# Kernel optimization log

Measured on AMD Instinct MI355X. Metric: run time of the kernel, lower is better.

The kernel has to match this reference:

```python
import jax, jax.numpy as jnp
import numpy as np

EPS = 1e-6
QMAX = 127.0  # 8-bit absmax activation quantization (BitNet b1.58 style)


def _quant_weight(W):
    # ternary {-1,0,1} with per-tensor mean-abs scale
    scale = jnp.mean(jnp.abs(W))
    scale = jnp.maximum(scale, EPS)
    q = jnp.clip(jnp.round(W / scale), -1.0, 1.0)
    return q * scale  # dequantized ternary weight


def _quant_act(x):
    # per-token absmax 8-bit quantization over the feature dim
    s = QMAX / jnp.maximum(jnp.max(jnp.abs(x), axis=-1, keepdims=True), EPS)
    q = jnp.clip(jnp.round(x * s), -QMAX - 1.0, QMAX)
    return q / s  # dequantized activation


def setup_inputs() -> dict:
    key = jax.random.key(0)
    k1, k2 = jax.random.split(key)
    B, S, D_IN, D_OUT = 4, 2048, 4096, 4096
    x = jax.random.normal(k1, (B, S, D_IN), dtype=jnp.float32)
    # xavier-uniform-ish weight init
    limit = float(np.sqrt(6.0 / (D_IN + D_OUT)))
    W = jax.random.uniform(k2, (D_OUT, D_IN), dtype=jnp.float32, minval=-limit, maxval=limit)
    b = jnp.zeros((D_OUT,), dtype=jnp.float32)
    return {"x": x, "W": W, "b": b}


def reference(x, W, b):
    dqx = _quant_act(x)      # [B,S,Din]
    dqw = _quant_weight(W)   # [Dout,Din]
    # F.linear: x @ W.T + b
    out = jnp.einsum('bsd,od->bso', dqx, dqw) + b
    return out
```

## Files before the change

kernel.cpp:

```cpp
#include <hip/hip_runtime.h>
#include <hip/hip_bf16.h>
#include <stdint.h>
#include <stddef.h>

#define DIN   4096
#define DOUT  4096
#define MTOK  8192
#define NW4   4194304

typedef __attribute__((ext_vector_type(4))) int   i32x4;
typedef __attribute__((ext_vector_type(4))) float f32x4;

#define OFF_SUM 0
#define OFF_WS  8
#define OFF_F   256
#define OFF_QX  65536
#define OFF_QW  (65536 + 8192*4096)

__global__ __launch_bounds__(256) void k_sumabs(const float* __restrict__ W,
                                                double* __restrict__ sum) {
  int idx = blockIdx.x * 256 + threadIdx.x;
  const f32x4* W4 = (const f32x4*)W;
  double s = 0.0;
#pragma unroll
  for (int i = 0; i < 8; ++i) {
    f32x4 v = W4[idx + i * 524288];
    s += (double)fabsf(v[0]);
    s += (double)fabsf(v[1]);
    s += (double)fabsf(v[2]);
    s += (double)fabsf(v[3]);
  }
#pragma unroll
  for (int off = 32; off > 0; off >>= 1) s += __shfl_xor(s, off);
  __shared__ double wsum[4];
  int lane = threadIdx.x & 63, w = threadIdx.x >> 6;
  if (lane == 0) wsum[w] = s;
  __syncthreads();
  if (threadIdx.x == 0) atomicAdd(sum, wsum[0] + wsum[1] + wsum[2] + wsum[3]);
}

__global__ void k_wscale(const double* __restrict__ sum, float* __restrict__ wsc) {
  double mean = *sum / 16777216.0;
  float s = (float)mean;
  if (s < 1e-6f) s = 1e-6f;
  *wsc = s;
}

__global__ __launch_bounds__(256) void k_quantw(const float* __restrict__ W,
                                                const float* __restrict__ wsc,
                                                char* __restrict__ qW) {
  int idx = blockIdx.x * 256 + threadIdx.x;
  float s = *wsc;
  f32x4 v = ((const f32x4*)W)[idx];
  int q0 = (int)fminf(fmaxf(rintf(v[0] / s), -1.f), 1.f);
  int q1 = (int)fminf(fmaxf(rintf(v[1] / s), -1.f), 1.f);
  int q2 = (int)fminf(fmaxf(rintf(v[2] / s), -1.f), 1.f);
  int q3 = (int)fminf(fmaxf(rintf(v[3] / s), -1.f), 1.f);
  uint32_t packed = (uint32_t)(q0 & 255) | ((uint32_t)(q1 & 255) << 8) |
                    ((uint32_t)(q2 & 255) << 16) | ((uint32_t)(q3 & 255) << 24);
  ((uint32_t*)qW)[idx] = packed;
}

__global__ __launch_bounds__(256) void k_quantx(const float* __restrict__ x,
                                                const float* __restrict__ wsc,
                                                char* __restrict__ qX,
                                                float* __restrict__ f) {
  int tok = blockIdx.x;
  int t = threadIdx.x;
  const f32x4* xr = (const f32x4*)(x + (size_t)tok * DIN);
  f32x4 v[4];
  float m = 0.f;
#pragma unroll
  for (int i = 0; i < 4; ++i) {
    v[i] = xr[t + 256 * i];
    m = fmaxf(m, fmaxf(fmaxf(fabsf(v[i][0]), fabsf(v[i][1])),
                       fmaxf(fabsf(v[i][2]), fabsf(v[i][3]))));
  }
#pragma unroll
  for (int off = 32; off > 0; off >>= 1) m = fmaxf(m, __shfl_xor(m, off));
  __shared__ float wm[4];
  if ((t & 63) == 0) wm[t >> 6] = m;
  __syncthreads();
  m = fmaxf(fmaxf(wm[0], wm[1]), fmaxf(wm[2], wm[3]));
  m = fmaxf(m, 1e-6f);
  float s = 127.0f / m;
  uint32_t* qr = (uint32_t*)(qX + (size_t)tok * DIN);
#pragma unroll
  for (int i = 0; i < 4; ++i) {
    int q0 = (int)fminf(fmaxf(rintf(v[i][0] * s), -128.f), 127.f);
    int q1 = (int)fminf(fmaxf(rintf(v[i][1] * s), -128.f), 127.f);
    int q2 = (int)fminf(fmaxf(rintf(v[i][2] * s), -128.f), 127.f);
    int q3 = (int)fminf(fmaxf(rintf(v[i][3] * s), -128.f), 127.f);
    uint32_t packed = (uint32_t)(q0 & 255) | ((uint32_t)(q1 & 255) << 8) |
                      ((uint32_t)(q2 & 255) << 16) | ((uint32_t)(q3 & 255) << 24);
    qr[t + 256 * i] = packed;
  }
  if (t == 0) f[tok] = (*wsc) * (m / 127.0f);
}

#define BM 128
#define BN 128
#define BK 64

__device__ __forceinline__ void gload16(const void* g, void* l) {
  __builtin_amdgcn_global_load_lds(
      (const __attribute__((address_space(1))) void*)g,
      (__attribute__((address_space(3))) void*)l, 16, 0, 0);
}

__global__ __launch_bounds__(256) void k_gemm(const char* __restrict__ qX,
                                              const char* __restrict__ qW,
                                              const float* __restrict__ f,
                                              const float* __restrict__ bias,
                                              float* __restrict__ out) {
  int bid = blockIdx.x;
  int swz = (bid & 7) * 256 + (bid >> 3);
  int bmi = swz >> 5;
  int bni = swz & 31;
  int bm0 = bmi * BM, bn0 = bni * BN;

  __shared__ char smem[16384];

  const int t = threadIdx.x;
  const int lane = t & 63;
  const int w = t >> 6;
  const int wm = w >> 1, wn = w & 1;

  i32x4 acc[4][4] = {};

  const int rs = t >> 2;
  const int cs = (t & 3) << 4;
  const char* srcA = qX + (size_t)(bm0 + rs) * DIN + cs;
  const char* srcB = qW + (size_t)(bn0 + rs) * DIN + cs;
  char* dstA0 = smem + w * 1024;
  char* dstA1 = smem + 4096 + w * 1024;
  char* dstB0 = smem + 8192 + w * 1024;
  char* dstB1 = smem + 12288 + w * 1024;

  const char* baseA = smem + (size_t)(wm * 64 + (lane & 15)) * 64 + ((lane >> 4) << 4);
  const char* baseB = smem + 8192 + (size_t)(wn * 64 + (lane & 15)) * 64 + ((lane >> 4) << 4);

  for (int kt = 0; kt < DIN / BK; ++kt) {
    const int k0 = kt * BK;
    gload16(srcA + k0, dstA0);
    gload16(srcA + (size_t)64 * DIN + k0, dstA1);
    gload16(srcB + k0, dstB0);
    gload16(srcB + (size_t)64 * DIN + k0, dstB1);
    __syncthreads();

    i32x4 a[4], b[4];
#pragma unroll
    for (int i = 0; i < 4; ++i) a[i] = *(const i32x4*)(baseA + i * 16 * 64);
#pragma unroll
    for (int j = 0; j < 4; ++j) b[j] = *(const i32x4*)(baseB + j * 16 * 64);
#pragma unroll
    for (int i = 0; i < 4; ++i)
#pragma unroll
      for (int j = 0; j < 4; ++j)
        acc[i][j] = __builtin_amdgcn_mfma_i32_16x16x64_i8(a[i], b[j], acc[i][j], 0, 0, 0);
    __syncthreads();
  }

  const int col0 = bn0 + wn * 64 + (lane & 15);
  const int row0 = bm0 + wm * 64 + ((lane >> 4) << 2);
  float bj[4];
#pragma unroll
  for (int j = 0; j < 4; ++j) bj[j] = bias[col0 + j * 16];
#pragma unroll
  for (int i = 0; i < 4; ++i) {
#pragma unroll
    for (int q = 0; q < 4; ++q) {
      const int m = row0 + i * 16 + q;
      const float fm = f[m];
      float* orow = out + (size_t)m * DOUT;
#pragma unroll
      for (int j = 0; j < 4; ++j)
        orow[col0 + j * 16] = (float)acc[i][j][q] * fm + bj[j];
    }
  }
}

extern "C" void kernel_launch(void* const* d_in, const int* in_sizes, int n_in,
                              void* d_out, int out_size, void* d_ws, size_t ws_size,
                              hipStream_t stream) {
  const float* x    = (const float*)d_in[0];
  const float* W    = (const float*)d_in[1];
  const float* bias = (const float*)d_in[2];
  float* out = (float*)d_out;
  char* ws = (char*)d_ws;

  double* sum = (double*)(ws + OFF_SUM);
  float* wsc  = (float*)(ws + OFF_WS);
  float* f    = (float*)(ws + OFF_F);
  char* qX    = ws + OFF_QX;
  char* qW    = ws + OFF_QW;

  hipMemsetAsync(d_ws, 0, 256, stream);
  k_sumabs<<<2048, 256, 0, stream>>>(W, sum);
  k_wscale<<<1, 1, 0, stream>>>(sum, wsc);
  k_quantw<<<16384, 256, 0, stream>>>(W, wsc, qW);
  k_quantx<<<8192, 256, 0, stream>>>(x, wsc, qX, f);
  k_gemm<<<2048, 256, 0, stream>>>(qX, qW, f, bias, out);
}
```

Baseline: 450.0 us.

## Merge quant kernels, pre-tile int8 operands, and pipeline a 256x256 int8 GEMM

Replaces the separate weight-scale, weight-quant and activation-quant kernels with one k_quant kernel. It folds in the weight-scale computation and writes qX and qW in a pre-tiled 16-row by 64-byte layout, so each GEMM stage is a contiguous 1 KB load per wave. The GEMM moves to 512-thread blocks with 256x256 output tiles and a 4-deep LDS ring buffer filled by global_load_lds. It uses vmcnt-based waits, a single barrier per k-step, MFMA priority hints and an XCD-aware block mapping, and applies the weight scale in the epilogue. The aim is fewer launches, more operand reuse and better load/compute overlap, at the cost of 128 KB of LDS per block and more registers per thread.

Result: no change. 450.1 us (+0.0%).

```diff
diff --git a/kernel.cpp b/kernel.cpp
--- a/kernel.cpp
+++ b/kernel.cpp
@@ -3,19 +3,19 @@
 #include <stdint.h>
 #include <stddef.h>
 
-#define DIN   4096
-#define DOUT  4096
-#define MTOK  8192
-#define NW4   4194304
+#define DIN  4096
+#define MTOK 8192
+#define NOUT 4096
+#define KT   64
 
 typedef __attribute__((ext_vector_type(4))) int   i32x4;
 typedef __attribute__((ext_vector_type(4))) float f32x4;
 
 #define OFF_SUM 0
-#define OFF_WS  8
 #define OFF_F   256
 #define OFF_QX  65536
-#define OFF_QW  (65536 + 8192*4096)
+#define OFF_QW  (65536 + (size_t)MTOK*DIN)
+
 
 __global__ __launch_bounds__(256) void k_sumabs(const float* __restrict__ W,
                                                 double* __restrict__ sum) {
@@ -25,10 +25,8 @@
 #pragma unroll
   for (int i = 0; i < 8; ++i) {
     f32x4 v = W4[idx + i * 524288];
-    s += (double)fabsf(v[0]);
-    s += (double)fabsf(v[1]);
-    s += (double)fabsf(v[2]);
-    s += (double)fabsf(v[3]);
+    s += (double)fabsf(v[0]) + (double)fabsf(v[1]) +
+         (double)fabsf(v[2]) + (double)fabsf(v[3]);
   }
 #pragma unroll
   for (int off = 32; off > 0; off >>= 1) s += __shfl_xor(s, off);
@@ -39,68 +37,88 @@
   if (threadIdx.x == 0) atomicAdd(sum, wsum[0] + wsum[1] + wsum[2] + wsum[3]);
 }
 
-__global__ void k_wscale(const double* __restrict__ sum, float* __restrict__ wsc) {
-  double mean = *sum / 16777216.0;
-  float s = (float)mean;
-  if (s < 1e-6f) s = 1e-6f;
-  *wsc = s;
-}
-
-__global__ __launch_bounds__(256) void k_quantw(const float* __restrict__ W,
-                                                const float* __restrict__ wsc,
-                                                char* __restrict__ qW) {
-  int idx = blockIdx.x * 256 + threadIdx.x;
-  float s = *wsc;
-  f32x4 v = ((const f32x4*)W)[idx];
-  int q0 = (int)fminf(fmaxf(rintf(v[0] / s), -1.f), 1.f);
-  int q1 = (int)fminf(fmaxf(rintf(v[1] / s), -1.f), 1.f);
-  int q2 = (int)fminf(fmaxf(rintf(v[2] / s), -1.f), 1.f);
-  int q3 = (int)fminf(fmaxf(rintf(v[3] / s), -1.f), 1.f);
-  uint32_t packed = (uint32_t)(q0 & 255) | ((uint32_t)(q1 & 255) << 8) |
-                    ((uint32_t)(q2 & 255) << 16) | ((uint32_t)(q3 & 255) << 24);
-  ((uint32_t*)qW)[idx] = packed;
-}
-
-__global__ __launch_bounds__(256) void k_quantx(const float* __restrict__ x,
-                                                const float* __restrict__ wsc,
-                                                char* __restrict__ qX,
-                                                float* __restrict__ f) {
-  int tok = blockIdx.x;
-  int t = threadIdx.x;
-  const f32x4* xr = (const f32x4*)(x + (size_t)tok * DIN);
-  f32x4 v[4];
-  float m = 0.f;
-#pragma unroll
-  for (int i = 0; i < 4; ++i) {
-    v[i] = xr[t + 256 * i];
-    m = fmaxf(m, fmaxf(fmaxf(fabsf(v[i][0]), fabsf(v[i][1])),
-                       fmaxf(fabsf(v[i][2]), fabsf(v[i][3]))));
-  }
-#pragma unroll
-  for (int off = 32; off > 0; off >>= 1) m = fmaxf(m, __shfl_xor(m, off));
-  __shared__ float wm[4];
-  if ((t & 63) == 0) wm[t >> 6] = m;
+__global__ __launch_bounds__(256) void k_quant(const float* __restrict__ x,
+                                               const float* __restrict__ W,
+                                               const double* __restrict__ sum,
+                                               char* __restrict__ qX,
+                                               char* __restrict__ qW,
+                                               float* __restrict__ f) {
+  __shared__ float sval[16];
+  __shared__ float red[16][4];
+  const int blk = blockIdx.x;
+  const int t = threadIdx.x;
+  const bool isW = (blk < 256);
+  const float* src;
+  char* dst;
+  if (isW) {
+    src = W + (size_t)blk * 16 * DIN;
+    dst = qW + (size_t)blk * 65536;
+  } else {
+    src = x + (size_t)(blk - 256) * 16 * DIN;
+    dst = qX + (size_t)(blk - 256) * 65536;
+  }
+  float lo, hi;
+  if (isW) {
+    if (t < 16) {
+      float s = (float)(*sum * (1.0 / 16777216.0));
+      if (s < 1e-6f) s = 1e-6f;
+      sval[t] = s;
+    }
+    lo = -1.f; hi = 1.f;
+  } else {
+    const f32x4* sv = (const f32x4*)src;
+    float rmax[16];
+#pragma unroll
+    for (int r = 0; r < 16; ++r) rmax[r] = 0.f;
+#pragma unroll
+    for (int i = 0; i < 64; ++i) {
+      f32x4 v = sv[i * 256 + t];
+      float mm = fmaxf(fmaxf(fabsf(v[0]), fabsf(v[1])),
+                       fmaxf(fabsf(v[2]), fabsf(v[3])));
+      rmax[i >> 2] = fmaxf(rmax[i >> 2], mm);
+    }
+    const int lane = t & 63, w = t >> 6;
+#pragma unroll
+    for (int r = 0; r < 16; ++r) {
+      float v = rmax[r];
+#pragma unroll
+      for (int off = 32; off > 0; off >>= 1) v = fmaxf(v, __shfl_xor(v, off));
+      if (lane == 0) red[r][w] = v;
+    }
+    __syncthreads();
+    if (t < 16) {
+      float m = fmaxf(fmaxf(red[t][0], red[t][1]), fmaxf(red[t][2], red[t][3]));
+      m = fmaxf(m, 1e-6f);
+      sval[t] = 127.0f / m;
+      f[(blk - 256) * 16 + t] = m * (1.0f / 127.0f);
+    }
+    lo = -128.f; hi = 127.f;
+  }
   __syncthreads();
-  m = fmaxf(fmaxf(wm[0], wm[1]), fmaxf(wm[2], wm[3]));
-  m = fmaxf(m, 1e-6f);
-  float s = 127.0f / m;
-  uint32_t* qr = (uint32_t*)(qX + (size_t)tok * DIN);
-#pragma unroll
-  for (int i = 0; i < 4; ++i) {
-    int q0 = (int)fminf(fmaxf(rintf(v[i][0] * s), -128.f), 127.f);
-    int q1 = (int)fminf(fmaxf(rintf(v[i][1] * s), -128.f), 127.f);
-    int q2 = (int)fminf(fmaxf(rintf(v[i][2] * s), -128.f), 127.f);
-    int q3 = (int)fminf(fmaxf(rintf(v[i][3] * s), -128.f), 127.f);
-    uint32_t packed = (uint32_t)(q0 & 255) | ((uint32_t)(q1 & 255) << 8) |
-                      ((uint32_t)(q2 & 255) << 16) | ((uint32_t)(q3 & 255) << 24);
-    qr[t + 256 * i] = packed;
-  }
-  if (t == 0) f[tok] = (*wsc) * (m / 127.0f);
-}
-
-#define BM 128
-#define BN 128
-#define BK 64
+#pragma unroll 4
+  for (int i = 0; i < 64; ++i) {
+    const int o = i * 1024 + t * 4;
+    const int row = (t >> 2) & 15;
+    const int k = i * 64 + (t >> 6) * 16 + (t & 3) * 4;
+    f32x4 v = *(const f32x4*)(src + (size_t)row * DIN + k);
+    float s = sval[row];
+    int q0, q1, q2, q3;
+    if (isW) {
+      q0 = (int)fminf(fmaxf(rintf(v[0] / s), lo), hi);
+      q1 = (int)fminf(fmaxf(rintf(v[1] / s), lo), hi);
+      q2 = (int)fminf(fmaxf(rintf(v[2] / s), lo), hi);
+      q3 = (int)fminf(fmaxf(rintf(v[3] / s), lo), hi);
+    } else {
+      q0 = (int)fminf(fmaxf(rintf(v[0] * s), lo), hi);
+      q1 = (int)fminf(fmaxf(rintf(v[1] * s), lo), hi);
+      q2 = (int)fminf(fmaxf(rintf(v[2] * s), lo), hi);
+      q3 = (int)fminf(fmaxf(rintf(v[3] * s), lo), hi);
+    }
+    uint32_t pk = (uint32_t)(q0 & 255) | ((uint32_t)(q1 & 255) << 8) |
+                  ((uint32_t)(q2 & 255) << 16) | ((uint32_t)(q3 & 255) << 24);
+    *(uint32_t*)(dst + o) = pk;
+  }
+}
 
 __device__ __forceinline__ void gload16(const void* g, void* l) {
   __builtin_amdgcn_global_load_lds(
@@ -108,76 +126,98 @@
       (__attribute__((address_space(3))) void*)l, 16, 0, 0);
 }
 
-__global__ __launch_bounds__(256) void k_gemm(const char* __restrict__ qX,
-                                              const char* __restrict__ qW,
-                                              const float* __restrict__ f,
-                                              const float* __restrict__ bias,
-                                              float* __restrict__ out) {
-  int bid = blockIdx.x;
-  int swz = (bid & 7) * 256 + (bid >> 3);
-  int bmi = swz >> 5;
-  int bni = swz & 31;
-  int bm0 = bmi * BM, bn0 = bni * BN;
-
-  __shared__ char smem[16384];
+__global__ __launch_bounds__(512, 2) void k_gemm(const char* __restrict__ qX,
+                                                 const char* __restrict__ qW,
+                                                 const float* __restrict__ f,
+                                                 const double* __restrict__ sum,
+                                                 const float* __restrict__ bias,
+                                                 float* __restrict__ out) {
+  const int bid = blockIdx.x;
+  const int xcd = bid & 7, slot = bid >> 3;
+  const int pass = slot >> 5, q = slot & 31;
+  const int mm = q >> 3, nn = q & 7;
+  const int pm = xcd >> 1, pn = xcd & 1;
+  const int bmi = pass * 16 + pm * 4 + mm;
+  const int bni = pn * 8 + nn;
+  const int mt0 = bmi * 16;
+  const int nt0 = bni * 16;
+
+  __shared__ __align__(16) char lds[4][2][16384];
 
   const int t = threadIdx.x;
   const int lane = t & 63;
   const int w = t >> 6;
-  const int wm = w >> 1, wn = w & 1;
-
-  i32x4 acc[4][4] = {};
-
-  const int rs = t >> 2;
-  const int cs = (t & 3) << 4;
-  const char* srcA = qX + (size_t)(bm0 + rs) * DIN + cs;
-  const char* srcB = qW + (size_t)(bn0 + rs) * DIN + cs;
-  char* dstA0 = smem + w * 1024;
-  char* dstA1 = smem + 4096 + w * 1024;
-  char* dstB0 = smem + 8192 + w * 1024;
-  char* dstB1 = smem + 12288 + w * 1024;
-
-  const char* baseA = smem + (size_t)(wm * 64 + (lane & 15)) * 64 + ((lane >> 4) << 4);
-  const char* baseB = smem + 8192 + (size_t)(wn * 64 + (lane & 15)) * 64 + ((lane >> 4) << 4);
-
-  for (int kt = 0; kt < DIN / BK; ++kt) {
-    const int k0 = kt * BK;
-    gload16(srcA + k0, dstA0);
-    gload16(srcA + (size_t)64 * DIN + k0, dstA1);
-    gload16(srcB + k0, dstB0);
-    gload16(srcB + (size_t)64 * DIN + k0, dstB1);
-    __syncthreads();
-
-    i32x4 a[4], b[4];
-#pragma unroll
-    for (int i = 0; i < 4; ++i) a[i] = *(const i32x4*)(baseA + i * 16 * 64);
-#pragma unroll
-    for (int j = 0; j < 4; ++j) b[j] = *(const i32x4*)(baseB + j * 16 * 64);
-#pragma unroll
-    for (int i = 0; i < 4; ++i)
+  const int wm = w >> 2, wn = w & 3;
+
+  const char* gA0 = qX + ((size_t)(mt0 + w) * 64) * 1024 + lane * 16;
+  const char* gA1 = qX + ((size_t)(mt0 + w + 8) * 64) * 1024 + lane * 16;
+  const char* gB0 = qW + ((size_t)(nt0 + w) * 64) * 1024 + lane * 16;
+  const char* gB1 = qW + ((size_t)(nt0 + w + 8) * 64) * 1024 + lane * 16;
+
+#define STAGE(buf, kt) do {                                     \
+    gload16(gA0 + (size_t)(kt) * 1024, &lds[buf][0][w * 1024]);        \
+    gload16(gA1 + (size_t)(kt) * 1024, &lds[buf][0][(w + 8) * 1024]);  \
+    gload16(gB0 + (size_t)(kt) * 1024, &lds[buf][1][w * 1024]);        \
+    gload16(gB1 + (size_t)(kt) * 1024, &lds[buf][1][(w + 8) * 1024]);  \
+  } while (0)
+
+  i32x4 acc[8][4] = {};
+
+  auto compute = [&](int buf) {
+    const char* bA = &lds[buf][0][wm * 8192 + lane * 16];
+    const char* bB = &lds[buf][1][wn * 4096 + lane * 16];
+    i32x4 a[8], b[4];
+#pragma unroll
+    for (int i = 0; i < 8; ++i) a[i] = *(const i32x4*)(bA + i * 1024);
+#pragma unroll
+    for (int j = 0; j < 4; ++j) b[j] = *(const i32x4*)(bB + j * 1024);
+    __builtin_amdgcn_s_setprio(1);
+#pragma unroll
+    for (int i = 0; i < 8; ++i)
 #pragma unroll
       for (int j = 0; j < 4; ++j)
         acc[i][j] = __builtin_amdgcn_mfma_i32_16x16x64_i8(a[i], b[j], acc[i][j], 0, 0, 0);
-    __syncthreads();
-  }
-
-  const int col0 = bn0 + wn * 64 + (lane & 15);
-  const int row0 = bm0 + wm * 64 + ((lane >> 4) << 2);
+    __builtin_amdgcn_s_setprio(0);
+  };
+
+  STAGE(0, 0);
+  STAGE(1, 1);
+  for (int kt = 0; kt < KT - 2; ++kt) {
+    STAGE((kt + 2) & 3, kt + 2);
+    asm volatile("s_waitcnt vmcnt(8)" ::: "memory");
+    __builtin_amdgcn_s_barrier();
+    asm volatile("" ::: "memory");
+    compute(kt & 3);
+  }
+  asm volatile("s_waitcnt vmcnt(4)" ::: "memory");
+  __builtin_amdgcn_s_barrier();
+  asm volatile("" ::: "memory");
+  compute((KT - 2) & 3);
+  asm volatile("s_waitcnt vmcnt(0)" ::: "memory");
+  __builtin_amdgcn_s_barrier();
+  asm volatile("" ::: "memory");
+  compute((KT - 1) & 3);
+
+  float wsc = (float)(*sum * (1.0 / 16777216.0));
+  if (wsc < 1e-6f) wsc = 1e-6f;
+  const int col0 = bni * 256 + wn * 64 + (lane & 15);
+  const int row0 = bmi * 256 + wm * 128 + ((lane >> 4) << 2);
   float bj[4];
 #pragma unroll
   for (int j = 0; j < 4; ++j) bj[j] = bias[col0 + j * 16];
 #pragma unroll
-  for (int i = 0; i < 4; ++i) {
-#pragma unroll
-    for (int q = 0; q < 4; ++q) {
-      const int m = row0 + i * 16 + q;
-      const float fm = f[m];
-      float* orow = out + (size_t)m * DOUT;
+  for (int i = 0; i < 8; ++i) {
+#pragma unroll
+    for (int qr = 0; qr < 4; ++qr) {
+      const int m = row0 + i * 16 + qr;
+      const float fm = f[m] * wsc;
+      float* orow = out + (size_t)m * NOUT;
 #pragma unroll
       for (int j = 0; j < 4; ++j)
-        orow[col0 + j * 16] = (float)acc[i][j][q] * fm + bj[j];
-    }
-  }
+        orow[col0 + j * 16] = (float)acc[i][j][qr] * fm + bj[j];
+    }
+  }
+#undef STAGE
 }
 
 extern "C" void kernel_launch(void* const* d_in, const int* in_sizes, int n_in,
@@ -190,15 +230,12 @@
   char* ws = (char*)d_ws;
 
   double* sum = (double*)(ws + OFF_SUM);
-  float* wsc  = (float*)(ws + OFF_WS);
   float* f    = (float*)(ws + OFF_F);
   char* qX    = ws + OFF_QX;
   char* qW    = ws + OFF_QW;
 
   hipMemsetAsync(d_ws, 0, 256, stream);
   k_sumabs<<<2048, 256, 0, stream>>>(W, sum);
-  k_wscale<<<1, 1, 0, stream>>>(sum, wsc);
-  k_quantw<<<16384, 256, 0, stream>>>(W, wsc, qW);
-  k_quantx<<<8192, 256, 0, stream>>>(x, wsc, qX, f);
-  k_gemm<<<2048, 256, 0, stream>>>(qX, qW, f, bias, out);
-}
+  k_quant<<<768, 256, 0, stream>>>(x, W, sum, qX, qW, f);
+  k_gemm<<<512, 512, 0, stream>>>(qX, qW, f, sum, bias, out);
+}
```
